# Optimization experiments

Measured on AMD Instinct MI355X. Metric: run time of the kernel, lower is better.

Reference implementation:

```python
import jax, jax.numpy as jnp
import numpy as np

N = 200000   # nodes
R = 4        # relations
E = 1000000  # edges per relation
B = 1024     # graphs in batch


def _graph_conv(h, s, d, ew, W, b):
    """DGL GraphConv, norm='both', optional edge_weight. h:[N,F_in] -> [N,F_out]."""
    n = h.shape[0]
    ones = jnp.ones(s.shape[0], dtype=h.dtype)
    out_deg = jnp.clip(jax.ops.segment_sum(ones, s, num_segments=n), 1.0)
    in_deg = jnp.clip(jax.ops.segment_sum(ones, d, num_segments=n), 1.0)
    hs = h * jax.lax.rsqrt(out_deg)[:, None]          # src-side norm
    m = hs[s]                                         # gather: [E, F_in]
    if ew is not None:
        m = m * ew[:, None]
    agg = jax.ops.segment_sum(m, d, num_segments=n)   # scatter-sum: [N, F_in]
    rst = agg * jax.lax.rsqrt(in_deg)[:, None]        # dst-side norm
    return rst @ W + b


def _hetero_layer(h, src, dst, ew, W, b):
    out = None
    for r in range(R):
        ewr = None if ew is None else ew[r]
        o = _graph_conv(h, src[r], dst[r], ewr, W[r], b[r])
        out = o if out is None else out + o
    return out


def setup_inputs() -> dict:
    key = jax.random.key(0)
    ks = jax.random.split(key, 10)
    feat = jax.random.normal(ks[0], (N, 2), dtype=jnp.float32)
    src = jax.random.randint(ks[1], (R, E), 0, N, dtype=jnp.int32)
    dst = jax.random.randint(ks[2], (R, E), 0, N, dtype=jnp.int32)
    ew = jax.random.uniform(ks[3], (R, E), dtype=jnp.float32)
    graph_ids = jnp.sort(jax.random.randint(ks[4], (N,), 0, B, dtype=jnp.int32))
    W1 = jax.random.normal(ks[5], (R, 2, 16), dtype=jnp.float32) * 0.5
    b1 = jnp.zeros((R, 16), dtype=jnp.float32)
    W2 = jax.random.normal(ks[6], (R, 16, 16), dtype=jnp.float32) * 0.25
    b2 = jnp.zeros((R, 16), dtype=jnp.float32)
    Wc = jax.random.normal(ks[7], (16, 2), dtype=jnp.float32) * 0.25
    bc = jnp.zeros((2,), dtype=jnp.float32)
    return {"feat": feat, "src": src, "dst": dst, "ew": ew,
            "graph_ids": graph_ids, "W1": W1, "b1": b1,
            "W2": W2, "b2": b2, "Wc": Wc, "bc": bc}


def reference(feat, src, dst, ew, graph_ids, W1, b1, W2, b2, Wc, bc):
    # layer 1: per-relation weighted GraphConv, summed over relations
    h = _hetero_layer(feat, src, dst, ew, W1, b1)
    h = jax.nn.relu(h)
    # layer 2: no edge weights (kwargs not forwarded in original code)
    h = _hetero_layer(h, src, dst, None, W2, b2)
    # mean_nodes per graph in the batch
    sums = jax.ops.segment_sum(h, graph_ids, num_segments=B)          # [B,16]
    cnts = jax.ops.segment_sum(jnp.ones((N,), h.dtype), graph_ids, num_segments=B)
    hg = sums / jnp.clip(cnts, 1.0)[:, None]
    return hg @ Wc + bc                                               # [B,2]
```

## Files before the change

### kernel.cpp

```cpp
#include <hip/hip_runtime.h>
#include <hip/hip_fp16.h>

#define NN 200000
#define RR 4
#define EE 1000000
#define BB 1024
#define RN (RR*NN)

#define BSH 7
#define BSZ 128
#define NB 1563
#define RK (RR*NB)
#define CSH 12
#define CNODES 4096
#define CC 49
#define CAPC 21504
#define EPB 8192
#define SBT 1024
#define BPR ((EE + EPB - 1) / EPB)
#define GSLOTS 32
#define CAPB 1024

#define SRC_OF(u)  (((u) >> 7) & 0x3FFFF)
#define DL_OF(u)   ((int)((u) & 127))
#define DEG_OF(u)  ((u) >> 25)

#define OFF_POOL   0
#define OFF_CNT    (OFF_POOL + BB*16)
#define OFF_GCS    (OFF_CNT + BB)
#define OFF_GCD    (OFF_GCS + RR*CC)
#define OFF_GFIN   (OFF_GCD + RR*CC)
#define ZERO_UNITS (OFF_GFIN + RK)
#define OFF_DEGB   ZERO_UNITS
#define OFF_INVI   (OFF_DEGB + RN/4)
#define OFF_RW16   (OFF_INVI + RN)
#define OFF_AGG1   (OFF_RW16 + RN/2)
#define OFF_SBC    OFF_AGG1
#define OFF_H1H    (OFF_AGG1 + RN*2)
#define OFF_KWCL   (OFF_H1H + NN*8)
#define OFF_KWCE   (OFF_KWCL + RR*CC*CAPC)
#define OFF_KW4    (OFF_KWCE + RR*CC*CAPC/2)


__global__ __launch_bounds__(SBT) void k_part(const int* __restrict__ src,
                                              const int* __restrict__ dst,
                                              const float* __restrict__ ew,
                                              int* __restrict__ gcs,
                                              int* __restrict__ gcd,
                                              unsigned short* __restrict__ sbc,
                                              unsigned* __restrict__ kwcL,
                                              unsigned short* __restrict__ kwcE) {
  __shared__ int cS[CC], bS[CC], lS[CC];
  __shared__ int cD[CC], bD[CC], lD[CC];
  int t = threadIdx.x, r = blockIdx.y, c0 = blockIdx.x * EPB;
  if (t < CC) { cS[t] = 0; cD[t] = 0; }
  __syncthreads();
  for (int i = t; i < EPB; i += SBT) {
    int e = c0 + i;
    if (e < EE) {
      atomicAdd(&cS[src[r * EE + e] >> CSH], 1);
      atomicAdd(&cD[dst[r * EE + e] >> CSH], 1);
    }
  }
  __syncthreads();
  if (t < CC) {
    int v = cS[t]; bS[t] = v ? atomicAdd(&gcs[r * CC + t], v) : 0; lS[t] = 0;
    int w = cD[t]; bD[t] = w ? atomicAdd(&gcd[r * CC + t], w) : 0; lD[t] = 0;
  }
  __syncthreads();
  for (int i = t; i < EPB; i += SBT) {
    int e = c0 + i;
    if (e < EE) {
      int idx = r * EE + e;
      int s = src[idx], d = dst[idx];
      int cs = s >> CSH;
      int offs = bS[cs] + atomicAdd(&lS[cs], 1);
      if (offs < CAPC)
        sbc[(size_t)(r * CC + cs) * CAPC + offs] = (unsigned short)(s & (CNODES - 1));
      int cd = d >> CSH;
      int offd = bD[cd] + atomicAdd(&lD[cd], 1);
      if (offd < CAPC) {
        size_t stD = (size_t)(r * CC + cd) * CAPC;
        kwcL[stD + offd] = (unsigned)(d & (CNODES - 1)) | ((unsigned)s << 12);
        kwcE[stD + offd] = __half_as_ushort(__float2half_rn(ew[idx]));
      }
    }
  }
}

__global__ __launch_bounds__(1024) void k_fineS(const unsigned short* __restrict__ sbc,
                                                const int* __restrict__ gcs,
                                                unsigned char* __restrict__ degb) {
  __shared__ int h[CNODES];
  int t = threadIdx.x, c = blockIdx.x, r = blockIdx.y;
  int kc = r * CC + c;
  size_t st = (size_t)kc * CAPC;
  int m = min(gcs[kc], CAPC);
  for (int i = t; i < CNODES; i += 1024) h[i] = 0;
  __syncthreads();
  for (int i = t; i < m; i += 1024) atomicAdd(&h[sbc[st + i]], 1);
  __syncthreads();
  int n0 = c * CNODES;
  for (int i = t; i < CNODES; i += 1024) {
    int n = n0 + i;
    if (n < NN) degb[r * NN + n] = (unsigned char)min(max(h[i], 1), 63);
  }
}

__global__ __launch_bounds__(1024) void k_fineD(const unsigned* __restrict__ kwcL,
                                                const unsigned short* __restrict__ kwcE,
                                                const int* __restrict__ gcd,
                                                const unsigned char* __restrict__ degb,
                                                const float* __restrict__ feat,
                                                unsigned* __restrict__ kw4,
                                                int* __restrict__ gfin,
                                                float* __restrict__ invi,
                                                unsigned short* __restrict__ rw16,
                                                float* __restrict__ agg1) {
  __shared__ int h[CNODES];
  __shared__ float la[CNODES * 2];
  __shared__ int s4[1024];
  __shared__ int sfb[33];
  int t = threadIdx.x, c = blockIdx.x, r = blockIdx.y;
  int kc = r * CC + c;
  size_t stc = (size_t)kc * CAPC;
  int nrec = min(gcd[kc], CAPC);
  for (int i = t; i < CNODES; i += 1024) h[i] = 0;
  for (int i = t; i < CNODES * 2; i += 1024) la[i] = 0.f;
  __syncthreads();
  for (int i = t; i < nrec; i += 1024) atomicAdd(&h[kwcL[stc + i] & (CNODES - 1)], 1);
  __syncthreads();
  int a0 = h[4 * t], a1 = h[4 * t + 1], a2 = h[4 * t + 2], a3 = h[4 * t + 3];
  int tot = a0 + a1 + a2 + a3;
  s4[t] = tot;
  __syncthreads();
  for (int off = 1; off < 1024; off <<= 1) {
    int v = (t >= off) ? s4[t - off] : 0;
    __syncthreads();
    s4[t] += v;
    __syncthreads();
  }
  int base = s4[t] - tot;
  if ((t & 31) == 0) sfb[t >> 5] = base;
  if (t == 1023) sfb[32] = s4[1023];
  __syncthreads();
  int n0 = c * CNODES;
  int e0 = base, e1 = base + a0, e2 = e1 + a1, e3 = e2 + a2;
  {
    int cl = 4 * t;
    int sb = sfb[cl >> 7];
    int n = n0 + cl;
    if (n < NN)     { invi[r*NN+n]   = rsqrtf((float)max(a0,1)); rw16[r*NN+n]   = (unsigned short)min(e0-sb, CAPB); }
    if (n + 1 < NN) { invi[r*NN+n+1] = rsqrtf((float)max(a1,1)); rw16[r*NN+n+1] = (unsigned short)min(e1-sb, CAPB); }
    if (n + 2 < NN) { invi[r*NN+n+2] = rsqrtf((float)max(a2,1)); rw16[r*NN+n+2] = (unsigned short)min(e2-sb, CAPB); }
    if (n + 3 < NN) { invi[r*NN+n+3] = rsqrtf((float)max(a3,1)); rw16[r*NN+n+3] = (unsigned short)min(e3-sb, CAPB); }
  }
  if (t < 32) {
    int kb = c * 32 + t;
    if (kb < NB) gfin[r * NB + kb] = min(sfb[t + 1] - sfb[t], CAPB);
  }
  __syncthreads();
  h[4 * t] = e0; h[4 * t + 1] = e1; h[4 * t + 2] = e2; h[4 * t + 3] = e3;
  __syncthreads();
  for (int i = t; i < nrec; i += 1024) {
    unsigned rc = kwcL[stc + i];
    int dcl = rc & (CNODES - 1);
    int s = rc >> 12;
    float ewf = __half2float(__ushort_as_half(kwcE[stc + i]));
    unsigned dg = degb[r * NN + s];
    float w1 = ewf * rsqrtf((float)dg);
    float2 fv = ((const float2*)feat)[s];
    atomicAdd(&la[dcl * 2],     fv.x * w1);
    atomicAdd(&la[dcl * 2 + 1], fv.y * w1);
    int pos = atomicAdd(&h[dcl], 1);
    int fb = dcl >> 7;
    int fpos = pos - sfb[fb];
    if (fpos < CAPB)
      kw4[(size_t)(r * NB + c * 32 + fb) * CAPB + fpos] =
          (rc & 127u) | ((unsigned)s << 7) | (dg << 25);
  }
  __syncthreads();
  for (int i = t; i < CNODES; i += 1024) {
    int n = n0 + i;
    if (n < NN)
      ((float2*)agg1)[r * NN + n] = make_float2(la[i * 2], la[i * 2 + 1]);
  }
}

__device__ __forceinline__ unsigned pack2h(float a, float b) {
  __half2 h = __floats2half2_rn(a, b);
  return *reinterpret_cast<unsigned*>(&h);
}

__global__ __launch_bounds__(256) void k_l1b(const float* __restrict__ agg1,
                                             const float* __restrict__ invi,
                                             const float* __restrict__ W1,
                                             const float* __restrict__ b1,
                                             __half* __restrict__ h1h) {
  __shared__ float sW[RR * 2 * 16];
  __shared__ float sb[16];
  int t = threadIdx.x, b = blockIdx.x;
  if (t < RR * 2 * 16) sW[t] = W1[t];
  if (t < 16) {
    float s = 0.f;
    for (int r = 0; r < RR; r++) s += b1[r * 16 + t];
    sb[t] = s;
  }
  __syncthreads();
  int n = b * 256 + t;
  if (n >= NN) return;
  float acc[16];
#pragma unroll
  for (int j = 0; j < 16; j++) acc[j] = sb[j];
#pragma unroll
  for (int r = 0; r < RR; r++) {
    float iv = invi[r * NN + n];
    float2 a = ((const float2*)agg1)[r * NN + n];
    float a0 = a.x * iv, a1 = a.y * iv;
#pragma unroll
    for (int j = 0; j < 16; j++)
      acc[j] += a0 * sW[(r * 2 + 0) * 16 + j] + a1 * sW[(r * 2 + 1) * 16 + j];
  }
#pragma unroll
  for (int j = 0; j < 16; j++) acc[j] = fmaxf(acc[j], 0.f);
  uint4 u0, u1;
  u0.x = pack2h(acc[0], acc[1]);  u0.y = pack2h(acc[2], acc[3]);
  u0.z = pack2h(acc[4], acc[5]);  u0.w = pack2h(acc[6], acc[7]);
  u1.x = pack2h(acc[8], acc[9]);  u1.y = pack2h(acc[10], acc[11]);
  u1.z = pack2h(acc[12], acc[13]); u1.w = pack2h(acc[14], acc[15]);
  uint4* o = (uint4*)(h1h + (size_t)n * 16);
  o[0] = u0; o[1] = u1;
}

__device__ __forceinline__ void acc8(float* acc, uint4 u, float w) {
  float2 p;
  p = __half22float2(*(__half2*)&u.x); acc[0] += p.x * w; acc[1] += p.y * w;
  p = __half22float2(*(__half2*)&u.y); acc[2] += p.x * w; acc[3] += p.y * w;
  p = __half22float2(*(__half2*)&u.z); acc[4] += p.x * w; acc[5] += p.y * w;
  p = __half22float2(*(__half2*)&u.w); acc[6] += p.x * w; acc[7] += p.y * w;
}

__global__ __launch_bounds__(256) void k_l2(const unsigned* __restrict__ kw4,
                                            const int* __restrict__ gfin,
                                            const unsigned short* __restrict__ rw16,
                                            const __half* __restrict__ h1h,
                                            const float* __restrict__ invi,
                                            const float* __restrict__ W2,
                                            const int* __restrict__ gid,
                                            float* __restrict__ pool,
                                            float* __restrict__ cnt) {
  __shared__ float agg[BSZ * 17];
  __shared__ float sW[16 * 16];
  __shared__ int   sg[BSZ];
  __shared__ unsigned short srw[BSZ + 1];
  __shared__ float gslot[GSLOTS * 16];
  __shared__ int   cslot[GSLOTS];
  __shared__ int   present[GSLOTS];
  int t = threadIdx.x, b = blockIdx.x, r = blockIdx.y;
  int n0 = b << BSH;
  int k = r * NB + b;
  int m = min(gfin[k], CAPB);
  sW[t] = W2[r * 256 + t];
  if (t < GSLOTS) { cslot[t] = 0; present[t] = 0; }
  for (int i = t; i < GSLOTS * 16; i += 256) gslot[i] = 0.f;
  if (t < BSZ) {
    int n = n0 + t;
    srw[t] = (n < NN) ? rw16[r * NN + n] : (unsigned short)m;
  }
  if (t == BSZ) srw[BSZ] = (unsigned short)m;
  __syncthreads();
  const uint4* h4p = (const uint4*)h1h;
  const unsigned* rb = kw4 + (size_t)k * CAPB;
  int f8 = t & 1, g = t >> 1;
  int e = srw[g], en = srw[g + 1];
  float acc[8];
#pragma unroll
  for (int j = 0; j < 8; j++) acc[j] = 0.f;
  for (; e + 3 < en; e += 4) {
    unsigned r0 = rb[e], r1 = rb[e + 1], r2 = rb[e + 2], r3 = rb[e + 3];
    uint4 u0 = h4p[(size_t)SRC_OF(r0) * 2 + f8];
    uint4 u1 = h4p[(size_t)SRC_OF(r1) * 2 + f8];
    uint4 u2 = h4p[(size_t)SRC_OF(r2) * 2 + f8];
    uint4 u3 = h4p[(size_t)SRC_OF(r3) * 2 + f8];
    acc8(acc, u0, rsqrtf((float)DEG_OF(r0)));
    acc8(acc, u1, rsqrtf((float)DEG_OF(r1)));
    acc8(acc, u2, rsqrtf((float)DEG_OF(r2)));
    acc8(acc, u3, rsqrtf((float)DEG_OF(r3)));
  }
  for (; e < en; e++) {
    unsigned rr = rb[e];
    uint4 u = h4p[(size_t)SRC_OF(rr) * 2 + f8];
    acc8(acc, u, rsqrtf((float)DEG_OF(rr)));
  }
#pragma unroll
  for (int j = 0; j < 8; j++) agg[g * 17 + 8 * f8 + j] = acc[j];
  __syncthreads();
  int n = n0 + t;
  int g0 = gid[n0];
  bool valid = (t < BSZ) && (n < NN);
  float out[16];
#pragma unroll
  for (int j = 0; j < 16; j++) out[j] = 0.f;
  if (valid) {
    float iv = invi[r * NN + n];
#pragma unroll
    for (int kk = 0; kk < 16; kk++) {
      float a = agg[t * 17 + kk] * iv;
#pragma unroll
      for (int j = 0; j < 16; j++) out[j] += a * sW[kk * 16 + j];
    }
  }
  __syncthreads();
  if (t < BSZ) {
    sg[t] = valid ? (gid[n] - g0) : -1;
#pragma unroll
    for (int j = 0; j < 16; j++) agg[t * 17 + j] = out[j];
  }
  __syncthreads();
  {
    int f = t & 15, i0 = t >> 4;
    for (int i = i0; i < BSZ; i += 16) {
      int gsN = sg[i];
      if (gsN < 0) continue;
      float v = agg[i * 17 + f];
      if (gsN < GSLOTS) {
        atomicAdd(&gslot[gsN * 16 + f], v);
        if (f == 0) {
          present[gsN] = 1;
          if (r == 0) atomicAdd(&cslot[gsN], 1);
        }
      } else {
        atomicAdd(&pool[(g0 + gsN) * 16 + f], v);
        if (f == 0 && r == 0) atomicAdd(&cnt[g0 + gsN], 1.0f);
      }
    }
  }
  __syncthreads();
  if (t < GSLOTS * 16) {
    int gsN = t >> 4, f = t & 15;
    if (present[gsN]) atomicAdd(&pool[(g0 + gsN) * 16 + f], gslot[t]);
  }
  if (r == 0 && t < GSLOTS && cslot[t] > 0)
    atomicAdd(&cnt[g0 + t], (float)cslot[t]);
}

__global__ __launch_bounds__(256) void k_final(const float* __restrict__ pool,
                                               const float* __restrict__ cnt,
                                               const float* __restrict__ b2,
                                               const float* __restrict__ Wc,
                                               const float* __restrict__ bc,
                                               float* __restrict__ out) {
  int b = blockIdx.x * 256 + threadIdx.x;
  if (b >= BB) return;
  float c = cnt[b];
  float inv = 1.0f / fmaxf(c, 1.0f);
  float o0 = bc[0], o1 = bc[1];
#pragma unroll
  for (int j = 0; j < 16; j++) {
    float sb = 0.f;
    for (int r = 0; r < RR; r++) sb += b2[r * 16 + j];
    float v = (pool[b * 16 + j] + c * sb) * inv;
    o0 += v * Wc[j * 2 + 0];
    o1 += v * Wc[j * 2 + 1];
  }
  out[b * 2 + 0] = o0;
  out[b * 2 + 1] = o1;
}

extern "C" void kernel_launch(void* const* d_in, const int* in_sizes, int n_in,
                              void* d_out, int out_size, void* d_ws, size_t ws_size,
                              hipStream_t stream) {
  const float* feat = (const float*)d_in[0];
  const int*   src  = (const int*)d_in[1];
  const int*   dst  = (const int*)d_in[2];
  const float* ew   = (const float*)d_in[3];
  const int*   gid  = (const int*)d_in[4];
  const float* W1   = (const float*)d_in[5];
  const float* b1   = (const float*)d_in[6];
  const float* W2   = (const float*)d_in[7];
  const float* b2   = (const float*)d_in[8];
  const float* Wc   = (const float*)d_in[9];
  const float* bc   = (const float*)d_in[10];

  char* ws = (char*)d_ws;
  float* pool   = (float*)(ws + (size_t)OFF_POOL * 4);
  float* cnt    = (float*)(ws + (size_t)OFF_CNT  * 4);
  int*   gcs    = (int*)  (ws + (size_t)OFF_GCS  * 4);
  int*   gcd    = (int*)  (ws + (size_t)OFF_GCD  * 4);
  int*   gfin   = (int*)  (ws + (size_t)OFF_GFIN * 4);
  unsigned char*  degb = (unsigned char*) (ws + (size_t)OFF_DEGB * 4);
  float* invi   = (float*)(ws + (size_t)OFF_INVI * 4);
  unsigned short* rw16 = (unsigned short*)(ws + (size_t)OFF_RW16 * 4);
  float* agg1   = (float*)(ws + (size_t)OFF_AGG1 * 4);
  unsigned short* sbc  = (unsigned short*)(ws + (size_t)OFF_SBC * 4);
  __half* h1h   = (__half*)(ws + (size_t)OFF_H1H * 4);
  unsigned* kwcL = (unsigned*)(ws + (size_t)OFF_KWCL * 4);
  unsigned short* kwcE = (unsigned short*)(ws + (size_t)OFF_KWCE * 4);
  unsigned* kw4 = (unsigned*)(ws + (size_t)OFF_KW4 * 4);

  hipMemsetAsync(d_ws, 0, (size_t)ZERO_UNITS * 4, stream);

  k_part  <<<dim3(BPR, RR), SBT, 0, stream>>>(src, dst, ew, gcs, gcd, sbc, kwcL, kwcE);
  k_fineS <<<dim3(CC, RR), 1024, 0, stream>>>(sbc, gcs, degb);
  k_fineD <<<dim3(CC, RR), 1024, 0, stream>>>(kwcL, kwcE, gcd, degb, feat, kw4, gfin, invi, rw16, agg1);
  k_l1b   <<<(NN + 255) / 256, 256, 0, stream>>>(agg1, invi, W1, b1, h1h);
  k_l2    <<<dim3(NB, RR), 256, 0, stream>>>(kw4, gfin, rw16, h1h, invi, W2, gid, pool, cnt);
  k_final <<<(BB + 255) / 256, 256, 0, stream>>>(pool, cnt, b2, Wc, bc, (float*)d_out);
}
```

Measured before the change: 351.9 us.

## Shrink coarse bucket to 1024 nodes for more blocks in fine passes

Coarse destination/source buckets go from 4096 to 1024 nodes, giving 196 chunks per relation instead of 49. The fine histogram and CSR-building kernels now map one node per thread, which removes the 4-per-thread scan logic and gives four times as many blocks to fill the GPU. Per-bucket capacities shrink, which adds a risk of overflow truncation. More coarse buckets also mean more global atomics and scattered writes in the bucketing pass.

```diff
diff --git a/kernel.cpp b/kernel.cpp
--- a/kernel.cpp
+++ b/kernel.cpp
@@ -11,15 +11,15 @@
 #define BSZ 128
 #define NB 1563
 #define RK (RR*NB)
-#define CSH 12
-#define CNODES 4096
-#define CC 49
-#define CAPC 21504
+#define CSH 10
+#define CNODES 1024
+#define CC 196
+#define CAPC 5632
 #define EPB 8192
 #define SBT 1024
 #define BPR ((EE + EPB - 1) / EPB)
 #define GSLOTS 32
-#define CAPB 1024
+#define CAPB 896
 
 #define SRC_OF(u)  (((u) >> 7) & 0x3FFFF)
 #define DL_OF(u)   ((int)((u) & 127))
@@ -81,7 +81,7 @@
       int offd = bD[cd] + atomicAdd(&lD[cd], 1);
       if (offd < CAPC) {
         size_t stD = (size_t)(r * CC + cd) * CAPC;
-        kwcL[stD + offd] = (unsigned)(d & (CNODES - 1)) | ((unsigned)s << 12);
+        kwcL[stD + offd] = (unsigned)(d & (CNODES - 1)) | ((unsigned)s << CSH);
         kwcE[stD + offd] = __half_as_ushort(__float2half_rn(ew[idx]));
       }
     }
@@ -96,15 +96,12 @@
   int kc = r * CC + c;
   size_t st = (size_t)kc * CAPC;
   int m = min(gcs[kc], CAPC);
-  for (int i = t; i < CNODES; i += 1024) h[i] = 0;
+  h[t] = 0;
   __syncthreads();
   for (int i = t; i < m; i += 1024) atomicAdd(&h[sbc[st + i]], 1);
   __syncthreads();
-  int n0 = c * CNODES;
-  for (int i = t; i < CNODES; i += 1024) {
-    int n = n0 + i;
-    if (n < NN) degb[r * NN + n] = (unsigned char)min(max(h[i], 1), 63);
-  }
+  int n = c * CNODES + t;
+  if (n < NN) degb[r * NN + n] = (unsigned char)min(max(h[t], 1), 63);
 }
 
 __global__ __launch_bounds__(1024) void k_fineD(const unsigned* __restrict__ kwcL,
@@ -120,19 +117,17 @@
   __shared__ int h[CNODES];
   __shared__ float la[CNODES * 2];
   __shared__ int s4[1024];
-  __shared__ int sfb[33];
+  __shared__ int sfb[9];
   int t = threadIdx.x, c = blockIdx.x, r = blockIdx.y;
   int kc = r * CC + c;
   size_t stc = (size_t)kc * CAPC;
   int nrec = min(gcd[kc], CAPC);
-  for (int i = t; i < CNODES; i += 1024) h[i] = 0;
-  for (int i = t; i < CNODES * 2; i += 1024) la[i] = 0.f;
+  h[t] = 0; la[t] = 0.f; la[t + CNODES] = 0.f;
   __syncthreads();
   for (int i = t; i < nrec; i += 1024) atomicAdd(&h[kwcL[stc + i] & (CNODES - 1)], 1);
   __syncthreads();
-  int a0 = h[4 * t], a1 = h[4 * t + 1], a2 = h[4 * t + 2], a3 = h[4 * t + 3];
-  int tot = a0 + a1 + a2 + a3;
-  s4[t] = tot;
+  int cntt = h[t];
+  s4[t] = cntt;
   __syncthreads();
   for (int off = 1; off < 1024; off <<= 1) {
     int v = (t >= off) ? s4[t - off] : 0;
@@ -140,32 +135,30 @@
     s4[t] += v;
     __syncthreads();
   }
-  int base = s4[t] - tot;
-  if ((t & 31) == 0) sfb[t >> 5] = base;
-  if (t == 1023) sfb[32] = s4[1023];
+  int base = s4[t] - cntt;
+  if ((t & 127) == 0) sfb[t >> 7] = base;
+  if (t == 1023) sfb[8] = s4[1023];
   __syncthreads();
   int n0 = c * CNODES;
-  int e0 = base, e1 = base + a0, e2 = e1 + a1, e3 = e2 + a2;
   {
-    int cl = 4 * t;
-    int sb = sfb[cl >> 7];
-    int n = n0 + cl;
-    if (n < NN)     { invi[r*NN+n]   = rsqrtf((float)max(a0,1)); rw16[r*NN+n]   = (unsigned short)min(e0-sb, CAPB); }
-    if (n + 1 < NN) { invi[r*NN+n+1] = rsqrtf((float)max(a1,1)); rw16[r*NN+n+1] = (unsigned short)min(e1-sb, CAPB); }
-    if (n + 2 < NN) { invi[r*NN+n+2] = rsqrtf((float)max(a2,1)); rw16[r*NN+n+2] = (unsigned short)min(e2-sb, CAPB); }
-    if (n + 3 < NN) { invi[r*NN+n+3] = rsqrtf((float)max(a3,1)); rw16[r*NN+n+3] = (unsigned short)min(e3-sb, CAPB); }
-  }
-  if (t < 32) {
-    int kb = c * 32 + t;
+    int sb = sfb[t >> 7];
+    int n = n0 + t;
+    if (n < NN) {
+      invi[r * NN + n] = rsqrtf((float)max(cntt, 1));
+      rw16[r * NN + n] = (unsigned short)min(base - sb, CAPB);
+    }
+  }
+  if (t < 8) {
+    int kb = c * 8 + t;
     if (kb < NB) gfin[r * NB + kb] = min(sfb[t + 1] - sfb[t], CAPB);
   }
   __syncthreads();
-  h[4 * t] = e0; h[4 * t + 1] = e1; h[4 * t + 2] = e2; h[4 * t + 3] = e3;
+  h[t] = base;
   __syncthreads();
   for (int i = t; i < nrec; i += 1024) {
     unsigned rc = kwcL[stc + i];
     int dcl = rc & (CNODES - 1);
-    int s = rc >> 12;
+    int s = rc >> CSH;
     float ewf = __half2float(__ushort_as_half(kwcE[stc + i]));
     unsigned dg = degb[r * NN + s];
     float w1 = ewf * rsqrtf((float)dg);
@@ -176,14 +169,14 @@
     int fb = dcl >> 7;
     int fpos = pos - sfb[fb];
     if (fpos < CAPB)
-      kw4[(size_t)(r * NB + c * 32 + fb) * CAPB + fpos] =
+      kw4[(size_t)(r * NB + c * 8 + fb) * CAPB + fpos] =
           (rc & 127u) | ((unsigned)s << 7) | (dg << 25);
   }
   __syncthreads();
-  for (int i = t; i < CNODES; i += 1024) {
-    int n = n0 + i;
+  {
+    int n = n0 + t;
     if (n < NN)
-      ((float2*)agg1)[r * NN + n] = make_float2(la[i * 2], la[i * 2 + 1]);
+      ((float2*)agg1)[r * NN + n] = make_float2(la[t * 2], la[t * 2 + 1]);
   }
 }
 
```

Measured after the change: 351.9 us. No clear change (-0.0%).
